# Optimization experiments

Measured on AMD Instinct MI355X. Metric: run time of the kernel, lower is better.

## Reference

```python
import jax, jax.numpy as jnp
import numpy as np

B, CIN, COUT, K, S, P, D = 4, 128, 128, 3, 1, 1, 1
H = W = 96
MASK_SCALE = 2.0


def setup_inputs() -> dict:
    key = jax.random.key(0)
    k1, k2, k3, k4 = jax.random.split(key, 4)
    x = jax.random.normal(k1, (B, CIN, H, W), jnp.float32)
    weight = jax.random.normal(k2, (COUT, CIN, K, K), jnp.float32) * 0.05
    bias = jax.random.normal(k3, (COUT,), jnp.float32) * 0.05
    # conv_offset_mask: out_channels = deformable_groups*3*K*K = 27, no bias
    w_offmask = jax.random.normal(k4, (3 * K * K, CIN, K, K), jnp.float32) * 0.01
    return {"x": x, "weight": weight, "bias": bias, "w_offmask": w_offmask}


def _bilinear_gather(x, py, px):
    """x: [B,C,H,W]; py,px: [B,K2,Ho,Wo] float sample coords.
    Returns [B,C,K2,Ho,Wo], zero outside image (per-corner validity as in DCNv2)."""
    Bn, C, Hh, Ww = x.shape
    K2, Ho, Wo = py.shape[1], py.shape[2], py.shape[3]
    y0 = jnp.floor(py); x0 = jnp.floor(px)
    ly = py - y0; lx = px - x0
    y0i = y0.astype(jnp.int32); x0i = x0.astype(jnp.int32)
    y1i = y0i + 1; x1i = x0i + 1
    x_flat = x.reshape(Bn, C, Hh * Ww)

    def corner(yi, xi, w):
        valid = (yi >= 0) & (yi < Hh) & (xi >= 0) & (xi < Ww)
        yc = jnp.clip(yi, 0, Hh - 1)
        xc = jnp.clip(xi, 0, Ww - 1)
        idx = (yc * Ww + xc).reshape(Bn, K2 * Ho * Wo)
        v = jnp.take_along_axis(x_flat, idx[:, None, :], axis=2)  # [B,C,K2*Ho*Wo]
        v = v.reshape(Bn, C, K2, Ho, Wo)
        wv = (w * valid.astype(x.dtype))[:, None]  # [B,1,K2,Ho,Wo]
        return v * wv

    out = corner(y0i, x0i, (1 - ly) * (1 - lx))
    out = out + corner(y0i, x1i, (1 - ly) * lx)
    out = out + corner(y1i, x0i, ly * (1 - lx))
    out = out + corner(y1i, x1i, ly * lx)
    return out


def reference(x, weight, bias, w_offmask):
    K2 = K * K
    # offset/mask conv (standard conv, no bias)
    om = jax.lax.conv_general_dilated(
        x, w_offmask, window_strides=(S, S), padding=[(P, P), (P, P)],
        dimension_numbers=("NCHW", "OIHW", "NCHW"))  # [B, 3*K2, Ho, Wo]
    o1 = om[:, :K2]
    o2 = om[:, K2:2 * K2]
    mask = jax.nn.sigmoid(om[:, 2 * K2:]) * MASK_SCALE  # [B,K2,Ho,Wo]
    offset = jnp.concatenate([o1, o2], axis=1)  # [B,2*K2,Ho,Wo]

    Ho, Wo = om.shape[2], om.shape[3]
    ki, kj = jnp.meshgrid(jnp.arange(K), jnp.arange(K), indexing="ij")
    ki = ki.reshape(K2); kj = kj.reshape(K2)
    ho = jnp.arange(Ho); wo = jnp.arange(Wo)
    base_y = (ho[None, :] * S - P + ki[:, None] * D).astype(x.dtype)  # [K2,Ho]
    base_x = (wo[None, :] * S - P + kj[:, None] * D).astype(x.dtype)  # [K2,Wo]
    py = base_y[None, :, :, None] + o1  # [B,K2,Ho,Wo]
    px = base_x[None, :, None, :] + o2

    sampled = _bilinear_gather(x, py, px)            # [B,C,K2,Ho,Wo]
    sampled = sampled * mask[:, None]                # modulation
    wr = weight.reshape(COUT, CIN, K2)
    out = jnp.einsum("ock,bckhw->bohw", wr, sampled) + bias[None, :, None, None]
    return out, offset
```

## Files before the change

### kernel.cpp

```cpp
#include <hip/hip_runtime.h>
#include <math.h>

#define HH 96
#define WW 96
#define HW (96*96)
#define CIN_ 128
#define COUT_ 128
#define OUT_ELEMS (4*128*96*96)
#define TPX 48

#define XT_OFF   0u
#define WBF_OFF  9437184u
#define WOMB_OFF 9732096u

typedef __attribute__((ext_vector_type(8))) short short8v;
typedef __attribute__((ext_vector_type(4))) float float4v;

__device__ __forceinline__ unsigned short f2bf(float f) {
    unsigned u = __builtin_bit_cast(unsigned, f);
    u += 0x7FFFu + ((u >> 16) & 1u);
    return (unsigned short)(u >> 16);
}
__device__ __forceinline__ unsigned rneu(float f) {
    unsigned u = __builtin_bit_cast(unsigned, f);
    return u + 0x7FFFu + ((u >> 16) & 1u);
}
__device__ __forceinline__ unsigned pkbf(float hi, float lo) {
    return __builtin_amdgcn_perm(rneu(hi), rneu(lo), 0x07060302u);
}
__device__ __forceinline__ float bflo(unsigned u) {
    return __builtin_bit_cast(float, u << 16);
}
__device__ __forceinline__ float bfhi(unsigned u) {
    return __builtin_bit_cast(float, u & 0xffff0000u);
}

__global__ __launch_bounds__(256) void pre_kernel(
    const float* __restrict__ x, const float* __restrict__ w,
    const float* __restrict__ wom, unsigned short* __restrict__ xt,
    unsigned short* __restrict__ wbf, unsigned short* __restrict__ womb)
{
    __shared__ float tile[64][130];
    const int t = threadIdx.x;
    const int f = blockIdx.x;

    if (f < 576) {
        const int g  = (f & 7) * 72 + (f >> 3);
        const int b  = g / 144;
        const int p0 = (g - b * 144) * 64;
#pragma unroll
        for (int j = 0; j < 8; j++) {
            const int i  = j * 256 + t;
            const int c  = i >> 4;
            const int p4 = (i & 15) * 4;
            const float4 v = *(const float4*)(x + ((size_t)(b * CIN_ + c) * HW + p0 + p4));
            tile[p4 + 0][c] = v.x; tile[p4 + 1][c] = v.y;
            tile[p4 + 2][c] = v.z; tile[p4 + 3][c] = v.w;
        }
        __syncthreads();
#pragma unroll
        for (int j = 0; j < 8; j++) {
            const int i   = j * 256 + t;
            const int pxl = i >> 5;
            const int c4  = (i & 31) * 4;
            uint2 v;
            v.x = pkbf(tile[pxl][c4 + 1], tile[pxl][c4 + 0]);
            v.y = pkbf(tile[pxl][c4 + 3], tile[pxl][c4 + 2]);
            *(uint2*)(xt + ((size_t)(b * HW + p0 + pxl) * CIN_ + c4)) = v;
        }
    } else {
        const int i = (f - 576) * 256 + t;
        if (i < COUT_ * 1152) {
            const int oc = i / 1152, r = i - oc * 1152;
            const int kc = r >> 7, c = r & 127;
            wbf[i] = f2bf(w[(size_t)oc * 1152 + c * 9 + kc]);
        } else {
            const int i2 = i - COUT_ * 1152;
            if (i2 < 32 * 1152) {
                const int row = i2 / 1152, r = i2 - row * 1152;
                const int kc = r >> 7, c = r & 127;
                womb[i2] = (row < 27) ? f2bf(wom[(size_t)row * 1152 + c * 9 + kc]) : 0;
            }
        }
    }
}

__global__ __launch_bounds__(512, 6) void dconv_fused(
    const unsigned short* __restrict__ xt, const unsigned short* __restrict__ wbf,
    const unsigned short* __restrict__ womb, const float* __restrict__ bias,
    float* __restrict__ out, float* __restrict__ off_out)
{
    __shared__ int smem[9600];
    int*   sprep  = smem;
    int*   btile0 = smem + 3456;
    int*   btile1 = smem + 6528;
    float* som    = (float*)btile0;

    const int t    = threadIdx.x;
    const int wave = __builtin_amdgcn_readfirstlane(t >> 6);
    const int lane = t & 63;
    const int quad = lane >> 4;
    const int m    = lane & 15;
    const int l32  = lane & 31;
    const int half = lane >> 5;

    const int f  = blockIdx.x;
    const int c  = (f & 7) * 96 + (f >> 3);
    const int b  = c / 192;
    const int p0 = (c - b * 192) * TPX;

    const unsigned short* xtb = xt + (size_t)b * HW * CIN_;

    if (wave < 6) {
        const int pxg = wave >> 1;
        const int mt  = wave & 1;
        const int pgl = pxg * 16 + m;
        const int pg  = p0 + pgl;
        const int h   = pg / 96;
        const int w   = pg - h * 96;

        float4v acc2;
#pragma unroll
        for (int r = 0; r < 4; r++) acc2[r] = 0.f;
        const short8v zerov = (short8v)0;

#pragma unroll
        for (int kc = 0; kc < 9; kc++) {
            const int ki = kc / 3, kj = kc - 3 * (kc / 3);
            const int y  = h + ki - 1, xx = w + kj - 1;
            const bool valid = ((unsigned)y < 96u) && ((unsigned)xx < 96u);
            const unsigned short* brow = xtb + (size_t)(y * 96 + xx) * CIN_ + quad * 8;
            const short* abase = (const short*)womb + (size_t)(mt * 16 + m) * 1152 + kc * 128 + quad * 8;
#pragma unroll
            for (int kst = 0; kst < 4; kst++) {
                const short8v bfv = valid ? *(const short8v*)(brow + kst * 32) : zerov;
                const short8v av  = *(const short8v*)(abase + kst * 32);
                acc2 = __builtin_amdgcn_mfma_f32_16x16x32_bf16(av, bfv, acc2, 0, 0, 0);
            }
        }
#pragma unroll
        for (int r = 0; r < 4; r++) {
            const int oc = mt * 16 + quad * 4 + r;
            if (oc < 27) som[oc * TPX + pgl] = acc2[r];
            if (oc < 18) off_out[(size_t)(b * 18 + oc) * HW + pg] = acc2[r];
        }
    }
    __syncthreads();

    if (t < 432) {
        const int kc  = t / 48;
        const int pxl = t - kc * 48;
        const int pg  = p0 + pxl;
        const int h   = pg / 96;
        const int w   = pg - h * 96;
        const int ki  = kc / 3, kj = kc - 3 * (kc / 3);

        const float o1 = som[kc * TPX + pxl];
        const float o2 = som[(9 + kc) * TPX + pxl];
        const float mr = som[(18 + kc) * TPX + pxl];
        const float mk = 2.f / (1.f + __expf(-mr));

        const float py = (float)(h - 1 + ki) + o1;
        const float px = (float)(w - 1 + kj) + o2;
        const float y0f = floorf(py), x0f = floorf(px);
        const float ly = py - y0f,    lx = px - x0f;
        const int y0 = (int)y0f, x0 = (int)x0f;
        const int y1 = y0 + 1,   x1 = x0 + 1;

        const float w00 = (1.f - ly) * (1.f - lx), w01 = (1.f - ly) * lx;
        const float w10 = ly * (1.f - lx),         w11 = ly * lx;

        const int yc0 = min(max(y0, 0), HH - 1), yc1 = min(max(y1, 0), HH - 1);
        const int xc0 = min(max(x0, 0), WW - 1), xc1 = min(max(x1, 0), WW - 1);
        const bool vy0 = (y0 >= 0) && (y0 < HH), vy1 = (y1 >= 0) && (y1 < HH);
        const bool vx0 = (x0 >= 0) && (x0 < WW), vx1 = (x1 >= 0) && (x1 < WW);

        sprep[t * 8 + 0] = yc0 * 96 + xc0;
        sprep[t * 8 + 1] = yc0 * 96 + xc1;
        sprep[t * 8 + 2] = yc1 * 96 + xc0;
        sprep[t * 8 + 3] = yc1 * 96 + xc1;
        sprep[t * 8 + 4] = __builtin_bit_cast(int, (vy0 && vx0) ? mk * w00 : 0.f);
        sprep[t * 8 + 5] = __builtin_bit_cast(int, (vy0 && vx1) ? mk * w01 : 0.f);
        sprep[t * 8 + 6] = __builtin_bit_cast(int, (vy1 && vx0) ? mk * w10 : 0.f);
        sprep[t * 8 + 7] = __builtin_bit_cast(int, (vy1 && vx1) ? mk * w11 : 0.f);
    }
    __syncthreads();

    uint2 gbuf[3][4];

#define ISSUE(SL, KCV, ITV) do {                                              \
    const int pxl_ = wave * 6 + (ITV) * 2 + half;                             \
    const int4 id4_ = *(const int4*)&sprep[((KCV) * 48 + pxl_) * 8];          \
    const unsigned co_ = (unsigned)l32 << 3;                                  \
    gbuf[SL][0] = *(const uint2*)((const char*)xtb + (((unsigned)id4_.x << 8) | co_)); \
    gbuf[SL][1] = *(const uint2*)((const char*)xtb + (((unsigned)id4_.y << 8) | co_)); \
    gbuf[SL][2] = *(const uint2*)((const char*)xtb + (((unsigned)id4_.z << 8) | co_)); \
    gbuf[SL][3] = *(const uint2*)((const char*)xtb + (((unsigned)id4_.w << 8) | co_)); \
} while (0)

#define COMBINE(SL, IV) do {                                                  \
    const int pxl_ = wave * 6 + (IV) * 2 + half;                              \
    const float4 w4_ = *(const float4*)&sprep[(kc * 48 + pxl_) * 8 + 4];      \
    const uint2 u0 = gbuf[SL][0], u1 = gbuf[SL][1];                           \
    const uint2 u2 = gbuf[SL][2], u3 = gbuf[SL][3];                           \
    const float v0 = w4_.x*bflo(u0.x) + w4_.y*bflo(u1.x) + w4_.z*bflo(u2.x) + w4_.w*bflo(u3.x); \
    const float v1 = w4_.x*bfhi(u0.x) + w4_.y*bfhi(u1.x) + w4_.z*bfhi(u2.x) + w4_.w*bfhi(u3.x); \
    const float v2 = w4_.x*bflo(u0.y) + w4_.y*bflo(u1.y) + w4_.z*bflo(u2.y) + w4_.w*bflo(u3.y); \
    const float v3 = w4_.x*bfhi(u0.y) + w4_.y*bfhi(u1.y) + w4_.z*bfhi(u2.y) + w4_.w*bfhi(u3.y); \
    uint2 o_;                                                                 \
    o_.x = pkbf(v1, v0);                                                      \
    o_.y = pkbf(v3, v2);                                                      \
    *(uint2*)&bt[pxl_ * 64 + (((l32 >> 1) ^ (pxl_ & 7)) << 2) + ((l32 & 1) << 1)] = o_; \
} while (0)

    float4v acc[3];
#pragma unroll
    for (int j = 0; j < 3; j++)
#pragma unroll
        for (int r = 0; r < 4; r++) acc[j][r] = 0.f;

    ISSUE(0, 0, 0);
    ISSUE(1, 0, 1);

    for (int kc = 0; kc < 9; kc++) {
        int* bt = (kc & 1) ? btile1 : btile0;

        ISSUE(2, kc, 2);
        COMBINE(0, 0);
        if (kc < 8) ISSUE(0, kc + 1, 0);
        COMBINE(1, 1);
        if (kc < 8) ISSUE(1, kc + 1, 1);
        COMBINE(2, 2);
        __syncthreads();

        const short* abase = (const short*)wbf + (size_t)(wave * 16 + m) * 1152 + kc * 128 + quad * 8;
#pragma unroll
        for (int kst = 0; kst < 4; kst++) {
            const short8v af = *(const short8v*)(abase + kst * 32);
#pragma unroll
            for (int nt = 0; nt < 3; nt++) {
                const int pxl = nt * 16 + m;
                const short8v bfv = *(const short8v*)((const short*)bt
                    + 2 * (pxl * 64 + (((kst * 4 + quad) ^ (m & 7)) << 2)));
                acc[nt] = __builtin_amdgcn_mfma_f32_16x16x32_bf16(af, bfv, acc[nt], 0, 0, 0);
            }
        }
    }
#undef ISSUE
#undef COMBINE

#pragma unroll
    for (int r = 0; r < 4; r++) {
        const int oc = wave * 16 + quad * 4 + r;
        const float bv = bias[oc];
#pragma unroll
        for (int nt = 0; nt < 3; nt++)
            out[(size_t)(b * COUT_ + oc) * HW + p0 + nt * 16 + m] = acc[nt][r] + bv;
    }
}

extern "C" void kernel_launch(void* const* d_in, const int* in_sizes, int n_in,
                              void* d_out, int out_size, void* d_ws, size_t ws_size,
                              hipStream_t stream) {
    const float* x      = (const float*)d_in[0];
    const float* weight = (const float*)d_in[1];
    const float* bias   = (const float*)d_in[2];
    const float* wom    = (const float*)d_in[3];

    float* out     = (float*)d_out;
    float* off_out = out + OUT_ELEMS;

    unsigned short* xtb  = (unsigned short*)((char*)d_ws + XT_OFF);
    unsigned short* wbf  = (unsigned short*)((char*)d_ws + WBF_OFF);
    unsigned short* womb = (unsigned short*)((char*)d_ws + WOMB_OFF);

    pre_kernel <<<dim3(1296), 256, 0, stream>>>(x, weight, wom, xtb, wbf, womb);
    dconv_fused<<<dim3(768),  512, 0, stream>>>(xtb, wbf, womb, bias, out, off_out);
}
```

Before: 159.0 us.

## Replace 512-thread block kernel with single-wave blocks gathering directly into MFMA registers

The fused deformable conv moves from 512-thread blocks covering 48 pixels to 64-thread single-wave blocks covering 16 pixels each. Each wave computes all 128 output channels with 8 accumulators. The bilinear-sampled B operand is built directly in registers and fed to MFMA, removing the LDS B-tile staging and the per-kc block barriers. The trade-off is that the weight matrix is reloaded from global/L2 by every wave with no cross-wave sharing, register pressure rises, and occupancy is limited by launch bounds of (64,3).

```diff
diff --git a/kernel.cpp b/kernel.cpp
--- a/kernel.cpp
+++ b/kernel.cpp
@@ -7,7 +7,6 @@
 #define CIN_ 128
 #define COUT_ 128
 #define OUT_ELEMS (4*128*96*96)
-#define TPX 48
 
 #define XT_OFF   0u
 #define WBF_OFF  9437184u
@@ -85,43 +84,38 @@
     }
 }
 
-__global__ __launch_bounds__(512, 6) void dconv_fused(
+__global__ __launch_bounds__(64, 3) void dconv_wave(
     const unsigned short* __restrict__ xt, const unsigned short* __restrict__ wbf,
     const unsigned short* __restrict__ womb, const float* __restrict__ bias,
     float* __restrict__ out, float* __restrict__ off_out)
 {
-    __shared__ int smem[9600];
-    int*   sprep  = smem;
-    int*   btile0 = smem + 3456;
-    int*   btile1 = smem + 6528;
-    float* som    = (float*)btile0;
-
-    const int t    = threadIdx.x;
-    const int wave = __builtin_amdgcn_readfirstlane(t >> 6);
-    const int lane = t & 63;
+    __shared__ int smem[1584];
+    int*   sprep = smem;
+    float* som   = (float*)(smem + 1152);
+
+    const int lane = threadIdx.x;
     const int quad = lane >> 4;
     const int m    = lane & 15;
-    const int l32  = lane & 31;
-    const int half = lane >> 5;
 
     const int f  = blockIdx.x;
-    const int c  = (f & 7) * 96 + (f >> 3);
-    const int b  = c / 192;
-    const int p0 = (c - b * 192) * TPX;
+    const int c  = (f & 7) * 288 + (f >> 3);
+    const int b  = c / 576;
+    const int p0 = (c - b * 576) * 16;
 
     const unsigned short* xtb = xt + (size_t)b * HW * CIN_;
-
-    if (wave < 6) {
-        const int pxg = wave >> 1;
-        const int mt  = wave & 1;
-        const int pgl = pxg * 16 + m;
-        const int pg  = p0 + pgl;
-        const int h   = pg / 96;
-        const int w   = pg - h * 96;
-
-        float4v acc2;
-#pragma unroll
-        for (int r = 0; r < 4; r++) acc2[r] = 0.f;
+    const char* xtB = (const char*)xtb;
+    const unsigned q16 = (unsigned)quad * 16u;
+
+    const int h  = p0 / 96;
+    const int w0 = p0 - h * 96;
+    const int w  = w0 + m;
+
+    {
+        float4v acc2[2];
+#pragma unroll
+        for (int i = 0; i < 2; i++)
+#pragma unroll
+            for (int r = 0; r < 4; r++) acc2[i][r] = 0.f;
         const short8v zerov = (short8v)0;
 
 #pragma unroll
@@ -130,40 +124,43 @@
             const int y  = h + ki - 1, xx = w + kj - 1;
             const bool valid = ((unsigned)y < 96u) && ((unsigned)xx < 96u);
             const unsigned short* brow = xtb + (size_t)(y * 96 + xx) * CIN_ + quad * 8;
-            const short* abase = (const short*)womb + (size_t)(mt * 16 + m) * 1152 + kc * 128 + quad * 8;
+            const short* a0 = (const short*)womb + (size_t)m * 1152 + kc * 128 + quad * 8;
 #pragma unroll
             for (int kst = 0; kst < 4; kst++) {
                 const short8v bfv = valid ? *(const short8v*)(brow + kst * 32) : zerov;
-                const short8v av  = *(const short8v*)(abase + kst * 32);
-                acc2 = __builtin_amdgcn_mfma_f32_16x16x32_bf16(av, bfv, acc2, 0, 0, 0);
+                const short8v av0 = *(const short8v*)(a0 + kst * 32);
+                const short8v av1 = *(const short8v*)(a0 + 16 * 1152 + kst * 32);
+                acc2[0] = __builtin_amdgcn_mfma_f32_16x16x32_bf16(av0, bfv, acc2[0], 0, 0, 0);
+                acc2[1] = __builtin_amdgcn_mfma_f32_16x16x32_bf16(av1, bfv, acc2[1], 0, 0, 0);
             }
         }
 #pragma unroll
         for (int r = 0; r < 4; r++) {
-            const int oc = mt * 16 + quad * 4 + r;
-            if (oc < 27) som[oc * TPX + pgl] = acc2[r];
-            if (oc < 18) off_out[(size_t)(b * 18 + oc) * HW + pg] = acc2[r];
+            const int oc0 = quad * 4 + r;
+            const int oc1 = 16 + quad * 4 + r;
+            som[oc0 * 16 + m] = acc2[0][r];
+            off_out[(size_t)(b * 18 + oc0) * HW + p0 + m] = acc2[0][r];
+            if (oc1 < 27) som[oc1 * 16 + m] = acc2[1][r];
+            if (oc1 < 18) off_out[(size_t)(b * 18 + oc1) * HW + p0 + m] = acc2[1][r];
         }
     }
     __syncthreads();
 
-    if (t < 432) {
-        const int kc  = t / 48;
-        const int pxl = t - kc * 48;
-        const int pg  = p0 + pxl;
-        const int h   = pg / 96;
-        const int w   = pg - h * 96;
-        const int ki  = kc / 3, kj = kc - 3 * (kc / 3);
-
-        const float o1 = som[kc * TPX + pxl];
-        const float o2 = som[(9 + kc) * TPX + pxl];
-        const float mr = som[(18 + kc) * TPX + pxl];
+    for (int it = lane; it < 144; it += 64) {
+        const int kc = it >> 4;
+        const int px = it & 15;
+        const int ki = kc / 3, kj = kc - 3 * (kc / 3);
+        const int wpx = w0 + px;
+
+        const float o1 = som[kc * 16 + px];
+        const float o2 = som[(9 + kc) * 16 + px];
+        const float mr = som[(18 + kc) * 16 + px];
         const float mk = 2.f / (1.f + __expf(-mr));
 
         const float py = (float)(h - 1 + ki) + o1;
-        const float px = (float)(w - 1 + kj) + o2;
-        const float y0f = floorf(py), x0f = floorf(px);
-        const float ly = py - y0f,    lx = px - x0f;
+        const float px_ = (float)(wpx - 1 + kj) + o2;
+        const float y0f = floorf(py), x0f = floorf(px_);
+        const float ly = py - y0f,    lx = px_ - x0f;
         const int y0 = (int)y0f, x0 = (int)x0f;
         const int y1 = y0 + 1,   x1 = x0 + 1;
 
@@ -175,87 +172,90 @@
         const bool vy0 = (y0 >= 0) && (y0 < HH), vy1 = (y1 >= 0) && (y1 < HH);
         const bool vx0 = (x0 >= 0) && (x0 < WW), vx1 = (x1 >= 0) && (x1 < WW);
 
-        sprep[t * 8 + 0] = yc0 * 96 + xc0;
-        sprep[t * 8 + 1] = yc0 * 96 + xc1;
-        sprep[t * 8 + 2] = yc1 * 96 + xc0;
-        sprep[t * 8 + 3] = yc1 * 96 + xc1;
-        sprep[t * 8 + 4] = __builtin_bit_cast(int, (vy0 && vx0) ? mk * w00 : 0.f);
-        sprep[t * 8 + 5] = __builtin_bit_cast(int, (vy0 && vx1) ? mk * w01 : 0.f);
-        sprep[t * 8 + 6] = __builtin_bit_cast(int, (vy1 && vx0) ? mk * w10 : 0.f);
-        sprep[t * 8 + 7] = __builtin_bit_cast(int, (vy1 && vx1) ? mk * w11 : 0.f);
+        sprep[it * 8 + 0] = yc0 * 96 + xc0;
+        sprep[it * 8 + 1] = yc0 * 96 + xc1;
+        sprep[it * 8 + 2] = yc1 * 96 + xc0;
+        sprep[it * 8 + 3] = yc1 * 96 + xc1;
+        sprep[it * 8 + 4] = __builtin_bit_cast(int, (vy0 && vx0) ? mk * w00 : 0.f);
+        sprep[it * 8 + 5] = __builtin_bit_cast(int, (vy0 && vx1) ? mk * w01 : 0.f);
+        sprep[it * 8 + 6] = __builtin_bit_cast(int, (vy1 && vx0) ? mk * w10 : 0.f);
+        sprep[it * 8 + 7] = __builtin_bit_cast(int, (vy1 && vx1) ? mk * w11 : 0.f);
     }
     __syncthreads();
 
-    uint2 gbuf[3][4];
-
-#define ISSUE(SL, KCV, ITV) do {                                              \
-    const int pxl_ = wave * 6 + (ITV) * 2 + half;                             \
-    const int4 id4_ = *(const int4*)&sprep[((KCV) * 48 + pxl_) * 8];          \
-    const unsigned co_ = (unsigned)l32 << 3;                                  \
-    gbuf[SL][0] = *(const uint2*)((const char*)xtb + (((unsigned)id4_.x << 8) | co_)); \
-    gbuf[SL][1] = *(const uint2*)((const char*)xtb + (((unsigned)id4_.y << 8) | co_)); \
-    gbuf[SL][2] = *(const uint2*)((const char*)xtb + (((unsigned)id4_.z << 8) | co_)); \
-    gbuf[SL][3] = *(const uint2*)((const char*)xtb + (((unsigned)id4_.w << 8) | co_)); \
+    const char* wbfB = (const char*)wbf + 2 * ((size_t)m * 1152 + quad * 8);
+
+#define CL4(D0, D1, D2, D3, ID, KST) do {                                     \
+    D0 = *(const uint4*)(xtB + (unsigned)(ID).x * 256u + q16 + (KST) * 64);   \
+    D1 = *(const uint4*)(xtB + (unsigned)(ID).y * 256u + q16 + (KST) * 64);   \
+    D2 = *(const uint4*)(xtB + (unsigned)(ID).z * 256u + q16 + (KST) * 64);   \
+    D3 = *(const uint4*)(xtB + (unsigned)(ID).w * 256u + q16 + (KST) * 64);   \
 } while (0)
 
-#define COMBINE(SL, IV) do {                                                  \
-    const int pxl_ = wave * 6 + (IV) * 2 + half;                              \
-    const float4 w4_ = *(const float4*)&sprep[(kc * 48 + pxl_) * 8 + 4];      \
-    const uint2 u0 = gbuf[SL][0], u1 = gbuf[SL][1];                           \
-    const uint2 u2 = gbuf[SL][2], u3 = gbuf[SL][3];                           \
-    const float v0 = w4_.x*bflo(u0.x) + w4_.y*bflo(u1.x) + w4_.z*bflo(u2.x) + w4_.w*bflo(u3.x); \
-    const float v1 = w4_.x*bfhi(u0.x) + w4_.y*bfhi(u1.x) + w4_.z*bfhi(u2.x) + w4_.w*bfhi(u3.x); \
-    const float v2 = w4_.x*bflo(u0.y) + w4_.y*bflo(u1.y) + w4_.z*bflo(u2.y) + w4_.w*bflo(u3.y); \
-    const float v3 = w4_.x*bfhi(u0.y) + w4_.y*bfhi(u1.y) + w4_.z*bfhi(u2.y) + w4_.w*bfhi(u3.y); \
-    uint2 o_;                                                                 \
-    o_.x = pkbf(v1, v0);                                                      \
-    o_.y = pkbf(v3, v2);                                                      \
-    *(uint2*)&bt[pxl_ * 64 + (((l32 >> 1) ^ (pxl_ & 7)) << 2) + ((l32 & 1) << 1)] = o_; \
+#define COMB(OUT, A0, A1, A2, A3, WV) do {                                    \
+    const float g0 = WV.x*bflo(A0.x)+WV.y*bflo(A1.x)+WV.z*bflo(A2.x)+WV.w*bflo(A3.x); \
+    const float g1 = WV.x*bfhi(A0.x)+WV.y*bfhi(A1.x)+WV.z*bfhi(A2.x)+WV.w*bfhi(A3.x); \
+    const float g2 = WV.x*bflo(A0.y)+WV.y*bflo(A1.y)+WV.z*bflo(A2.y)+WV.w*bflo(A3.y); \
+    const float g3 = WV.x*bfhi(A0.y)+WV.y*bfhi(A1.y)+WV.z*bfhi(A2.y)+WV.w*bfhi(A3.y); \
+    const float g4 = WV.x*bflo(A0.z)+WV.y*bflo(A1.z)+WV.z*bflo(A2.z)+WV.w*bflo(A3.z); \
+    const float g5 = WV.x*bfhi(A0.z)+WV.y*bfhi(A1.z)+WV.z*bfhi(A2.z)+WV.w*bfhi(A3.z); \
+    const float g6 = WV.x*bflo(A0.w)+WV.y*bflo(A1.w)+WV.z*bflo(A2.w)+WV.w*bflo(A3.w); \
+    const float g7 = WV.x*bfhi(A0.w)+WV.y*bfhi(A1.w)+WV.z*bfhi(A2.w)+WV.w*bfhi(A3.w); \
+    uint4 o_;                                                                 \
+    o_.x = pkbf(g1, g0); o_.y = pkbf(g3, g2);                                 \
+    o_.z = pkbf(g5, g4); o_.w = pkbf(g7, g6);                                 \
+    OUT = __builtin_bit_cast(short8v, o_);                                    \
 } while (0)
 
-    float4v acc[3];
-#pragma unroll
-    for (int j = 0; j < 3; j++)
-#pragma unroll
-        for (int r = 0; r < 4; r++) acc[j][r] = 0.f;
-
-    ISSUE(0, 0, 0);
-    ISSUE(1, 0, 1);
-
-    for (int kc = 0; kc < 9; kc++) {
-        int* bt = (kc & 1) ? btile1 : btile0;
-
-        ISSUE(2, kc, 2);
-        COMBINE(0, 0);
-        if (kc < 8) ISSUE(0, kc + 1, 0);
-        COMBINE(1, 1);
-        if (kc < 8) ISSUE(1, kc + 1, 1);
-        COMBINE(2, 2);
-        __syncthreads();
-
-        const short* abase = (const short*)wbf + (size_t)(wave * 16 + m) * 1152 + kc * 128 + quad * 8;
-#pragma unroll
-        for (int kst = 0; kst < 4; kst++) {
-            const short8v af = *(const short8v*)(abase + kst * 32);
-#pragma unroll
-            for (int nt = 0; nt < 3; nt++) {
-                const int pxl = nt * 16 + m;
-                const short8v bfv = *(const short8v*)((const short*)bt
-                    + 2 * (pxl * 64 + (((kst * 4 + quad) ^ (m & 7)) << 2)));
-                acc[nt] = __builtin_amdgcn_mfma_f32_16x16x32_bf16(af, bfv, acc[nt], 0, 0, 0);
-            }
-        }
-    }
-#undef ISSUE
-#undef COMBINE
-
-#pragma unroll
-    for (int r = 0; r < 4; r++) {
-        const int oc = wave * 16 + quad * 4 + r;
-        const float bv = bias[oc];
-#pragma unroll
-        for (int nt = 0; nt < 3; nt++)
-            out[(size_t)(b * COUT_ + oc) * HW + p0 + nt * 16 + m] = acc[nt][r] + bv;
+#define MMA8(BF, KST) do {                                                    \
+    _Pragma("unroll")                                                         \
+    for (int mt_ = 0; mt_ < 8; mt_++) {                                       \
+        const short8v af_ = *(const short8v*)(wbfB + 2 * (mt_ * 18432 + kck + (KST) * 32)); \
+        acc[mt_] = __builtin_amdgcn_mfma_f32_16x16x32_bf16(af_, BF, acc[mt_], 0, 0, 0); \
+    }                                                                         \
+} while (0)
+
+    float4v acc[8];
+#pragma unroll
+    for (int i = 0; i < 8; i++)
+#pragma unroll
+        for (int r = 0; r < 4; r++) acc[i][r] = 0.f;
+
+    int4   idc = *(const int4*)  &sprep[m * 8];
+    float4 wc  = *(const float4*)&sprep[m * 8 + 4];
+
+    uint4 ca0, ca1, ca2, ca3, cb0, cb1, cb2, cb3;
+    CL4(ca0, ca1, ca2, ca3, idc, 0);
+
+    for (int kc = 0; kc < 9; ++kc) {
+        const int kck = kc * 128;
+        const int nidx = (kc < 8) ? kc + 1 : kc;
+        const int4   idn = *(const int4*)  &sprep[(nidx * 16 + m) * 8];
+        const float4 wn  = *(const float4*)&sprep[(nidx * 16 + m) * 8 + 4];
+        short8v bf;
+
+        CL4(cb0, cb1, cb2, cb3, idc, 1);
+        COMB(bf, ca0, ca1, ca2, ca3, wc);  MMA8(bf, 0);
+        CL4(ca0, ca1, ca2, ca3, idc, 2);
+        COMB(bf, cb0, cb1, cb2, cb3, wc);  MMA8(bf, 1);
+        CL4(cb0, cb1, cb2, cb3, idc, 3);
+        COMB(bf, ca0, ca1, ca2, ca3, wc);  MMA8(bf, 2);
+        CL4(ca0, ca1, ca2, ca3, idn, 0);
+        COMB(bf, cb0, cb1, cb2, cb3, wc);  MMA8(bf, 3);
+
+        idc = idn; wc = wn;
+    }
+#undef CL4
+#undef COMB
+#undef MMA8
+
+#pragma unroll
+    for (int mt = 0; mt < 8; mt++) {
+#pragma unroll
+        for (int r = 0; r < 4; r++) {
+            const int oc = mt * 16 + quad * 4 + r;
+            out[(size_t)(b * COUT_ + oc) * HW + p0 + m] = acc[mt][r] + bias[oc];
+        }
     }
 }
 
@@ -274,6 +274,6 @@
     unsigned short* wbf  = (unsigned short*)((char*)d_ws + WBF_OFF);
     unsigned short* womb = (unsigned short*)((char*)d_ws + WOMB_OFF);
 
-    pre_kernel <<<dim3(1296), 256, 0, stream>>>(x, weight, wom, xtb, wbf, womb);
-    dconv_fused<<<dim3(768),  512, 0, stream>>>(xtb, wbf, womb, bias, out, off_out);
-}
+    pre_kernel<<<dim3(1296), 256, 0, stream>>>(x, weight, wom, xtb, wbf, womb);
+    dconv_wave<<<dim3(2304),  64, 0, stream>>>(xtb, wbf, womb, bias, out, off_out);
+}
```

Measured after the change: 210.9 us. 32.6% more time.
